# Optimization experiments

Hardware: AMD Instinct MI355X
Metric: run time of the kernel (lower is better)

The kernel has to match this reference:

```python
import jax, jax.numpy as jnp
import numpy as np

N = 2_000_000
FEAT = 83      # mat_feature_len
DIMF = 64      # dim_features
LAT = 32       # latent_dim
INIT_RANGE = 0.02
SHIFT_INIT = 0.001
EPS = 1e-12


def setup_inputs() -> dict:
    key = jax.random.key(0)
    ks = jax.random.split(key, 8)
    inputs = jax.random.normal(ks[0], (N, FEAT), dtype=jnp.float32)
    keep = jax.random.bernoulli(ks[1], 0.5, (N,))
    inputs = inputs * keep[:, None].astype(jnp.float32)
    shift = jnp.full((1,), SHIFT_INIT, dtype=jnp.float32)  # ZeroShift scalar
    W1 = jax.random.normal(ks[2], (FEAT, DIMF), dtype=jnp.float32) * INIT_RANGE
    b1 = jnp.zeros((DIMF,), dtype=jnp.float32)
    Wh0 = jax.random.normal(ks[3], (DIMF, LAT), dtype=jnp.float32) * INIT_RANGE
    bh0 = jnp.zeros((LAT,), dtype=jnp.float32)
    Wh1 = jax.random.normal(ks[4], (LAT, LAT), dtype=jnp.float32) * INIT_RANGE
    bh1 = jnp.zeros((LAT,), dtype=jnp.float32)
    return {"inputs": inputs, "shift": shift, "W1": W1, "b1": b1,
            "Wh0": Wh0, "bh0": bh0, "Wh1": Wh1, "bh1": bh1}


def reference(inputs, shift, W1, b1, Wh0, bh0, Wh1, bh1):
    # mask_zero: a material row is valid iff any feature is nonzero
    mask = jnp.any(inputs != 0, axis=-1)  # (N,)
    # Original gathers valid rows, runs MLP, scatters back (zeros elsewhere).
    # All ops are row-wise, so compute densely and zero masked rows — same math.
    x = inputs + shift                            # ZeroShift (scalar shift)
    x = jax.nn.relu(x @ W1 + b1)                  # dens_1 -> (N, DIMF)
    x = jax.nn.relu(x @ Wh0 + bh0)                # hidden 0 -> (N, LAT)
    x = jax.nn.relu(x @ Wh1 + bh1)                # hidden 1 -> (N, LAT)
    # UnifyVector: L2-normalize rows
    norm = jnp.sqrt(jnp.sum(x * x, axis=-1, keepdims=True))
    emb = x / jnp.maximum(norm, EPS)
    emb = emb * mask[:, None].astype(emb.dtype)   # scatter_nd equivalent
    return (emb, emb, emb)
```

## Files before the change

### kernel.cpp

```cpp
#include <hip/hip_runtime.h>

#define FEAT 83
#define DIMF 64
#define LAT  32
#define THREADS 256
#define RPB  128

typedef __attribute__((ext_vector_type(8))) short bf16x8;
typedef __attribute__((ext_vector_type(4))) float f32x4;
typedef __attribute__((ext_vector_type(4))) unsigned u32x4;

#define BT1H 0
#define BT1L 6144
#define BT2H 12288
#define BT2L 14336
#define BT3H 16384
#define BT3L 17408
#define WS_SHORTS 18432

#define SM_SHORTS 26880

__device__ __forceinline__ short f2b(float f) {
    unsigned u = __float_as_uint(f);
    u += 0x7fffu + ((u >> 16) & 1u);
    return (short)(u >> 16);
}
__device__ __forceinline__ float b2f(short h) {
    return __uint_as_float(((unsigned)(unsigned short)h) << 16);
}

__global__ void prep_weights(const float* __restrict__ W1,
                             const float* __restrict__ Wh0,
                             const float* __restrict__ Wh1,
                             short* __restrict__ ws)
{
    const int stride = gridDim.x * blockDim.x;
    const int tid = blockIdx.x * blockDim.x + threadIdx.x;
    for (int idx = tid; idx < 64 * 96; idx += stride) {
        int c = idx / 96, k = idx - c * 96;
        float w = (k < FEAT) ? W1[k * 64 + c] : 0.f;
        short hi = f2b(w);
        ws[BT1H + idx] = hi;
        ws[BT1L + idx] = f2b(w - b2f(hi));
    }
    for (int idx = tid; idx < 32 * 64; idx += stride) {
        int c = idx >> 6, k = idx & 63;
        float w = Wh0[k * 32 + c];
        short hi = f2b(w);
        ws[BT2H + idx] = hi;
        ws[BT2L + idx] = f2b(w - b2f(hi));
    }
    for (int idx = tid; idx < 32 * 32; idx += stride) {
        int c = idx >> 5, k = idx & 31;
        float w = Wh1[k * 32 + c];
        short hi = f2b(w);
        ws[BT3H + idx] = hi;
        ws[BT3L + idx] = f2b(w - b2f(hi));
    }
}

__device__ __forceinline__ void unpack8(const unsigned* p, bf16x8& hi, bf16x8& lo) {
    union { bf16x8 v; unsigned u[4]; } H, L;
    #pragma unroll
    for (int d = 0; d < 4; ++d) {
        H.u[d] = __builtin_amdgcn_perm(p[2 * d + 1], p[2 * d], 0x07060302u);
        L.u[d] = __builtin_amdgcn_perm(p[2 * d + 1], p[2 * d], 0x05040100u);
    }
    hi = H.v; lo = L.v;
}

__global__ __launch_bounds__(THREADS, 3)
void material_encoder_kernel(const float* __restrict__ inp,
                             const float* __restrict__ shiftp,
                             const short* __restrict__ ws,
                             const float* __restrict__ b1,
                             const float* __restrict__ bh0,
                             const float* __restrict__ bh1,
                             float* __restrict__ out,
                             int nrows)
{
    __shared__ __align__(16) short sm[SM_SHORTS];
    unsigned* scr = (unsigned*)((char*)sm + 36864) + (threadIdx.x >> 6) * 1024;
    float* maskf  = (float*)((char*)sm + 53248);

    const int t    = threadIdx.x;
    const int lane = t & 63;
    const int wv   = t >> 6;
    const int lr   = lane & 15;
    const int lq   = (lane >> 4) & 3;

    f32x4 wreg[9];
    {
        const f32x4* __restrict__ wsrc = (const f32x4*)ws;
        #pragma unroll
        for (int it = 0; it < 9; ++it) wreg[it] = wsrc[it * THREADS + t];
    }

    float bias1[4], bias2[2], bias3[2];
    #pragma unroll
    for (int n = 0; n < 4; ++n) bias1[n] = b1[lr + 16 * n];
    #pragma unroll
    for (int n = 0; n < 2; ++n) { bias2[n] = bh0[lr + 16 * n]; bias3[n] = bh1[lr + 16 * n]; }
    const float sh = shiftp[0];
    const int Rw = blockIdx.x * RPB + wv * 32;

    bf16x8 a1h[2][3], a1l[2][3];
    float nzm[2];
    #pragma unroll
    for (int m = 0; m < 2; ++m) {
        const float* __restrict__ xr = inp + (long long)(Rw + 16 * m + lr) * FEAT;
        float nz = 0.f;
        #pragma unroll
        for (int s = 0; s < 3; ++s) {
            const int k0 = 32 * s + 8 * lq;
            bf16x8 fh, fl;
            #pragma unroll
            for (int i = 0; i < 8; ++i) {
                const int kk = k0 + i;
                float x = 0.f;
                if (kk < FEAT) x = xr[kk];
                nz = fmaxf(nz, fabsf(x));
                const float xs = x + sh;
                const unsigned u = __float_as_uint(xs);
                fh[i] = (short)(u >> 16);
                fl[i] = f2b(xs - __uint_as_float(u & 0xffff0000u));
            }
            a1h[m][s] = fh;
            a1l[m][s] = fl;
        }
        nzm[m] = nz;
    }
    #pragma unroll
    for (int m = 0; m < 2; ++m) {
        nzm[m] = fmaxf(nzm[m], __shfl_xor(nzm[m], 16));
        nzm[m] = fmaxf(nzm[m], __shfl_xor(nzm[m], 32));
    }
    if (lq == 0) {
        maskf[wv * 32 + lr]      = nzm[0];
        maskf[wv * 32 + 16 + lr] = nzm[1];
    }

    {
        f32x4* wdst = (f32x4*)sm;
        #pragma unroll
        for (int it = 0; it < 9; ++it) wdst[it * THREADS + t] = wreg[it];
    }
    __syncthreads();

    f32x4 acc[2][4];
    #pragma unroll
    for (int m = 0; m < 2; ++m)
        #pragma unroll
        for (int n = 0; n < 4; ++n)
            acc[m][n] = (f32x4){bias1[n], bias1[n], bias1[n], bias1[n]};

    #pragma unroll
    for (int s = 0; s < 3; ++s)
        #pragma unroll
        for (int n = 0; n < 4; ++n) {
            bf16x8 bh = *(const bf16x8*)&sm[BT1H + (lr + 16 * n) * 96 + 32 * s + 8 * lq];
            bf16x8 bl = *(const bf16x8*)&sm[BT1L + (lr + 16 * n) * 96 + 32 * s + 8 * lq];
            #pragma unroll
            for (int m = 0; m < 2; ++m) {
                acc[m][n] = __builtin_amdgcn_mfma_f32_16x16x32_bf16(a1h[m][s], bh, acc[m][n], 0, 0, 0);
                acc[m][n] = __builtin_amdgcn_mfma_f32_16x16x32_bf16(a1l[m][s], bh, acc[m][n], 0, 0, 0);
                acc[m][n] = __builtin_amdgcn_mfma_f32_16x16x32_bf16(a1h[m][s], bl, acc[m][n], 0, 0, 0);
            }
        }

    f32x4 acc2[2][2];
    #pragma unroll
    for (int m = 0; m < 2; ++m)
        #pragma unroll
        for (int n = 0; n < 2; ++n)
            acc2[m][n] = (f32x4){bias2[n], bias2[n], bias2[n], bias2[n]};

    #pragma unroll
    for (int s = 0; s < 2; ++s) {
        #pragma unroll
        for (int m = 0; m < 2; ++m)
            #pragma unroll
            for (int np = 0; np < 2; ++np)
                #pragma unroll
                for (int r = 0; r < 4; ++r) {
                    const float hv = fmaxf(acc[m][2 * s + np][r], 0.f);
                    const unsigned u = __float_as_uint(hv);
                    const unsigned hiu = u & 0xffff0000u;
                    const unsigned lo16 =
                        (unsigned short)f2b(hv - __uint_as_float(hiu));
                    scr[(16 * m + 4 * lq + r) * 32 + lr + 16 * np] = hiu | lo16;
                }
        bf16x8 a2h[2], a2l[2];
        #pragma unroll
        for (int m = 0; m < 2; ++m) {
            unsigned p[8];
            *(u32x4*)&p[0] = *(const u32x4*)&scr[(lr + 16 * m) * 32 + 8 * lq];
            *(u32x4*)&p[4] = *(const u32x4*)&scr[(lr + 16 * m) * 32 + 8 * lq + 4];
            unpack8(p, a2h[m], a2l[m]);
        }
        #pragma unroll
        for (int n = 0; n < 2; ++n) {
            bf16x8 bh = *(const bf16x8*)&sm[BT2H + (lr + 16 * n) * 64 + 32 * s + 8 * lq];
            bf16x8 bl = *(const bf16x8*)&sm[BT2L + (lr + 16 * n) * 64 + 32 * s + 8 * lq];
            #pragma unroll
            for (int m = 0; m < 2; ++m) {
                acc2[m][n] = __builtin_amdgcn_mfma_f32_16x16x32_bf16(a2h[m], bh, acc2[m][n], 0, 0, 0);
                acc2[m][n] = __builtin_amdgcn_mfma_f32_16x16x32_bf16(a2l[m], bh, acc2[m][n], 0, 0, 0);
                acc2[m][n] = __builtin_amdgcn_mfma_f32_16x16x32_bf16(a2h[m], bl, acc2[m][n], 0, 0, 0);
            }
        }
    }

    f32x4 acc3[2][2];
    #pragma unroll
    for (int m = 0; m < 2; ++m)
        #pragma unroll
        for (int n = 0; n < 2; ++n)
            acc3[m][n] = (f32x4){bias3[n], bias3[n], bias3[n], bias3[n]};

    #pragma unroll
    for (int m = 0; m < 2; ++m)
        #pragma unroll
        for (int n = 0; n < 2; ++n)
            #pragma unroll
            for (int r = 0; r < 4; ++r) {
                const float gv = fmaxf(acc2[m][n][r], 0.f);
                const unsigned u = __float_as_uint(gv);
                const unsigned hiu = u & 0xffff0000u;
                const unsigned lo16 =
                    (unsigned short)f2b(gv - __uint_as_float(hiu));
                scr[(16 * m + 4 * lq + r) * 32 + lr + 16 * n] = hiu | lo16;
            }
    {
        bf16x8 a3h[2], a3l[2];
        #pragma unroll
        for (int m = 0; m < 2; ++m) {
            unsigned p[8];
            *(u32x4*)&p[0] = *(const u32x4*)&scr[(lr + 16 * m) * 32 + 8 * lq];
            *(u32x4*)&p[4] = *(const u32x4*)&scr[(lr + 16 * m) * 32 + 8 * lq + 4];
            unpack8(p, a3h[m], a3l[m]);
        }
        #pragma unroll
        for (int n = 0; n < 2; ++n) {
            bf16x8 bh = *(const bf16x8*)&sm[BT3H + (lr + 16 * n) * 32 + 8 * lq];
            bf16x8 bl = *(const bf16x8*)&sm[BT3L + (lr + 16 * n) * 32 + 8 * lq];
            #pragma unroll
            for (int m = 0; m < 2; ++m) {
                acc3[m][n] = __builtin_amdgcn_mfma_f32_16x16x32_bf16(a3h[m], bh, acc3[m][n], 0, 0, 0);
                acc3[m][n] = __builtin_amdgcn_mfma_f32_16x16x32_bf16(a3l[m], bh, acc3[m][n], 0, 0, 0);
                acc3[m][n] = __builtin_amdgcn_mfma_f32_16x16x32_bf16(a3h[m], bl, acc3[m][n], 0, 0, 0);
            }
        }
    }

    float er[2][2][4];
    float ssq[2][4];
    #pragma unroll
    for (int m = 0; m < 2; ++m)
        #pragma unroll
        for (int r = 0; r < 4; ++r) ssq[m][r] = 0.f;
    #pragma unroll
    for (int m = 0; m < 2; ++m)
        #pragma unroll
        for (int n = 0; n < 2; ++n)
            #pragma unroll
            for (int r = 0; r < 4; ++r) {
                float e = fmaxf(acc3[m][n][r], 0.f);
                er[m][n][r] = e;
                ssq[m][r] = fmaf(e, e, ssq[m][r]);
            }
    #pragma unroll
    for (int msk = 1; msk <= 8; msk <<= 1)
        #pragma unroll
        for (int m = 0; m < 2; ++m)
            #pragma unroll
            for (int r = 0; r < 4; ++r)
                ssq[m][r] += __shfl_xor(ssq[m][r], msk);

    const float* maskp = maskf + wv * 32;
    f32x4 mk[2];
    mk[0] = *(const f32x4*)&maskp[4 * lq];
    mk[1] = *(const f32x4*)&maskp[16 + 4 * lq];

    float sc[2][4];
    #pragma unroll
    for (int m = 0; m < 2; ++m)
        #pragma unroll
        for (int r = 0; r < 4; ++r)
            sc[m][r] = (mk[m][r] != 0.f) ? rsqrtf(fmaxf(ssq[m][r], 1e-24f)) : 0.f;

    const int osz = nrows * LAT;
    float* __restrict__ ob = out + (long long)Rw * LAT;
    #pragma unroll
    for (int m = 0; m < 2; ++m)
        #pragma unroll
        for (int r = 0; r < 4; ++r) {
            const int ro = (16 * m + 4 * lq + r) * LAT;
            #pragma unroll
            for (int n = 0; n < 2; ++n) {
                const float vv = er[m][n][r] * sc[m][r];
                const int cc = ro + lr + 16 * n;
                ob[cc]           = vv;
                ob[osz + cc]     = vv;
                ob[2 * osz + cc] = vv;
            }
        }
}

extern "C" void kernel_launch(void* const* d_in, const int* in_sizes, int n_in,
                              void* d_out, int out_size, void* d_ws, size_t ws_size,
                              hipStream_t stream) {
    const float* inp    = (const float*)d_in[0];
    const float* shiftp = (const float*)d_in[1];
    const float* W1     = (const float*)d_in[2];
    const float* b1     = (const float*)d_in[3];
    const float* Wh0    = (const float*)d_in[4];
    const float* bh0    = (const float*)d_in[5];
    const float* Wh1    = (const float*)d_in[6];
    const float* bh1    = (const float*)d_in[7];
    float* out = (float*)d_out;
    short* ws  = (short*)d_ws;

    const int nrows = in_sizes[0] / FEAT;
    const int blocks = nrows / RPB;

    prep_weights<<<dim3(24), dim3(THREADS), 0, stream>>>(W1, Wh0, Wh1, ws);
    material_encoder_kernel<<<dim3(blocks), dim3(THREADS), 0, stream>>>(
        inp, shiftp, ws, b1, bh0, bh1, out, nrows);
}
```

Baseline: 274.4 us.

## Stage input tile through LDS with coalesced vector loads before MFMA fragments

Each block now loads its 128x83 float input tile with contiguous 16-byte vector loads into registers, writes it to shared memory with the weights, and builds the bf16 hi/lo MFMA fragments from LDS. Previously each lane read its own row with strided scalar global loads. The per-wave scratch area now overlaps the input tile and the LDS footprint grows, so launch bounds drop from 3 to 2 blocks per SM, which lowers occupancy and latency hiding. Out-of-range feature indices are clamped to the last column instead of zeroed, which looks like it could put a nonzero value into the padded K slots; whether that changes the result depends on whether the padded weights are zero.

```diff
diff --git a/kernel.cpp b/kernel.cpp
--- a/kernel.cpp
+++ b/kernel.cpp
@@ -10,15 +10,16 @@
 typedef __attribute__((ext_vector_type(4))) float f32x4;
 typedef __attribute__((ext_vector_type(4))) unsigned u32x4;
 
-#define BT1H 0
-#define BT1L 6144
-#define BT2H 12288
-#define BT2L 14336
-#define BT3H 16384
-#define BT3L 17408
+#define WT1H 0
+#define WT1L 6144
+#define WT2H 12288
+#define WT2L 14336
+#define WT3H 16384
+#define WT3L 17408
 #define WS_SHORTS 18432
 
-#define SM_SHORTS 26880
+#define WOFF 21248
+#define SM_SHORTS 39936
 
 __device__ __forceinline__ short f2b(float f) {
     unsigned u = __float_as_uint(f);
@@ -40,22 +41,22 @@
         int c = idx / 96, k = idx - c * 96;
         float w = (k < FEAT) ? W1[k * 64 + c] : 0.f;
         short hi = f2b(w);
-        ws[BT1H + idx] = hi;
-        ws[BT1L + idx] = f2b(w - b2f(hi));
+        ws[WT1H + idx] = hi;
+        ws[WT1L + idx] = f2b(w - b2f(hi));
     }
     for (int idx = tid; idx < 32 * 64; idx += stride) {
         int c = idx >> 6, k = idx & 63;
         float w = Wh0[k * 32 + c];
         short hi = f2b(w);
-        ws[BT2H + idx] = hi;
-        ws[BT2L + idx] = f2b(w - b2f(hi));
+        ws[WT2H + idx] = hi;
+        ws[WT2L + idx] = f2b(w - b2f(hi));
     }
     for (int idx = tid; idx < 32 * 32; idx += stride) {
         int c = idx >> 5, k = idx & 31;
         float w = Wh1[k * 32 + c];
         short hi = f2b(w);
-        ws[BT3H + idx] = hi;
-        ws[BT3L + idx] = f2b(w - b2f(hi));
+        ws[WT3H + idx] = hi;
+        ws[WT3L + idx] = f2b(w - b2f(hi));
     }
 }
 
@@ -69,7 +70,7 @@
     hi = H.v; lo = L.v;
 }
 
-__global__ __launch_bounds__(THREADS, 3)
+__global__ __launch_bounds__(THREADS, 2)
 void material_encoder_kernel(const float* __restrict__ inp,
                              const float* __restrict__ shiftp,
                              const short* __restrict__ ws,
@@ -80,8 +81,9 @@
                              int nrows)
 {
     __shared__ __align__(16) short sm[SM_SHORTS];
-    unsigned* scr = (unsigned*)((char*)sm + 36864) + (threadIdx.x >> 6) * 1024;
-    float* maskf  = (float*)((char*)sm + 53248);
+    float* xt     = (float*)sm;
+    unsigned* scr = (unsigned*)((char*)sm + (threadIdx.x >> 6) * 10624);
+    float* maskf  = (float*)((char*)sm + 79360);
 
     const int t    = threadIdx.x;
     const int lane = t & 63;
@@ -89,6 +91,16 @@
     const int lr   = lane & 15;
     const int lq   = (lane >> 4) & 3;
 
+    f32x4 xreg[11];
+    {
+        const f32x4* __restrict__ src4 =
+            (const f32x4*)(inp + (long long)blockIdx.x * (RPB * FEAT));
+        #pragma unroll
+        for (int it = 0; it < 11; ++it) {
+            const int idx = it * THREADS + t;
+            if (idx < (RPB * FEAT / 4)) xreg[it] = src4[idx];
+        }
+    }
     f32x4 wreg[9];
     {
         const f32x4* __restrict__ wsrc = (const f32x4*)ws;
@@ -104,11 +116,24 @@
     const float sh = shiftp[0];
     const int Rw = blockIdx.x * RPB + wv * 32;
 
+    {
+        f32x4* xdst = (f32x4*)sm;
+        #pragma unroll
+        for (int it = 0; it < 11; ++it) {
+            const int idx = it * THREADS + t;
+            if (idx < (RPB * FEAT / 4)) xdst[idx] = xreg[it];
+        }
+        f32x4* wdst = (f32x4*)(sm + WOFF);
+        #pragma unroll
+        for (int it = 0; it < 9; ++it) wdst[it * THREADS + t] = wreg[it];
+    }
+    __syncthreads();
+
     bf16x8 a1h[2][3], a1l[2][3];
     float nzm[2];
     #pragma unroll
     for (int m = 0; m < 2; ++m) {
-        const float* __restrict__ xr = inp + (long long)(Rw + 16 * m + lr) * FEAT;
+        const float* __restrict__ xr = xt + (wv * 32 + 16 * m + lr) * FEAT;
         float nz = 0.f;
         #pragma unroll
         for (int s = 0; s < 3; ++s) {
@@ -116,9 +141,9 @@
             bf16x8 fh, fl;
             #pragma unroll
             for (int i = 0; i < 8; ++i) {
-                const int kk = k0 + i;
-                float x = 0.f;
-                if (kk < FEAT) x = xr[kk];
+                int kk = k0 + i;
+                kk = (kk < FEAT) ? kk : (FEAT - 1);
+                const float x = xr[kk];
                 nz = fmaxf(nz, fabsf(x));
                 const float xs = x + sh;
                 const unsigned u = __float_as_uint(xs);
@@ -140,13 +165,6 @@
         maskf[wv * 32 + 16 + lr] = nzm[1];
     }
 
-    {
-        f32x4* wdst = (f32x4*)sm;
-        #pragma unroll
-        for (int it = 0; it < 9; ++it) wdst[it * THREADS + t] = wreg[it];
-    }
-    __syncthreads();
-
     f32x4 acc[2][4];
     #pragma unroll
     for (int m = 0; m < 2; ++m)
@@ -158,8 +176,8 @@
     for (int s = 0; s < 3; ++s)
         #pragma unroll
         for (int n = 0; n < 4; ++n) {
-            bf16x8 bh = *(const bf16x8*)&sm[BT1H + (lr + 16 * n) * 96 + 32 * s + 8 * lq];
-            bf16x8 bl = *(const bf16x8*)&sm[BT1L + (lr + 16 * n) * 96 + 32 * s + 8 * lq];
+            bf16x8 bh = *(const bf16x8*)&sm[WOFF + WT1H + (lr + 16 * n) * 96 + 32 * s + 8 * lq];
+            bf16x8 bl = *(const bf16x8*)&sm[WOFF + WT1L + (lr + 16 * n) * 96 + 32 * s + 8 * lq];
             #pragma unroll
             for (int m = 0; m < 2; ++m) {
                 acc[m][n] = __builtin_amdgcn_mfma_f32_16x16x32_bf16(a1h[m][s], bh, acc[m][n], 0, 0, 0);
@@ -200,8 +218,8 @@
         }
         #pragma unroll
         for (int n = 0; n < 2; ++n) {
-            bf16x8 bh = *(const bf16x8*)&sm[BT2H + (lr + 16 * n) * 64 + 32 * s + 8 * lq];
-            bf16x8 bl = *(const bf16x8*)&sm[BT2L + (lr + 16 * n) * 64 + 32 * s + 8 * lq];
+            bf16x8 bh = *(const bf16x8*)&sm[WOFF + WT2H + (lr + 16 * n) * 64 + 32 * s + 8 * lq];
+            bf16x8 bl = *(const bf16x8*)&sm[WOFF + WT2L + (lr + 16 * n) * 64 + 32 * s + 8 * lq];
             #pragma unroll
             for (int m = 0; m < 2; ++m) {
                 acc2[m][n] = __builtin_amdgcn_mfma_f32_16x16x32_bf16(a2h[m], bh, acc2[m][n], 0, 0, 0);
@@ -242,8 +260,8 @@
         }
         #pragma unroll
         for (int n = 0; n < 2; ++n) {
-            bf16x8 bh = *(const bf16x8*)&sm[BT3H + (lr + 16 * n) * 32 + 8 * lq];
-            bf16x8 bl = *(const bf16x8*)&sm[BT3L + (lr + 16 * n) * 32 + 8 * lq];
+            bf16x8 bh = *(const bf16x8*)&sm[WOFF + WT3H + (lr + 16 * n) * 32 + 8 * lq];
+            bf16x8 bl = *(const bf16x8*)&sm[WOFF + WT3L + (lr + 16 * n) * 32 + 8 * lq];
             #pragma unroll
             for (int m = 0; m < 2; ++m) {
                 acc3[m][n] = __builtin_amdgcn_mfma_f32_16x16x32_bf16(a3h[m], bh, acc3[m][n], 0, 0, 0);
```

Result: slower. 283.7 us (+3.4%).
